# Optimization experiments

Measured on AMD Instinct MI355X. Metric: run time of the kernel, lower is better.

## Reference

```python
import jax, jax.numpy as jnp
import numpy as np

B, A = 65536, 32          # batch, n_agents
D, H1, H2, L = 4, 32, 32, 16  # local MLP dims
G_IN, G_H, G_OUT = 2 * L, 32, 2  # global MLP dims


def _lin_init(k, fan_in, fan_out):
    kw, kb = jax.random.split(k)
    s = 1.0 / np.sqrt(fan_in)
    W = jax.random.uniform(kw, (fan_in, fan_out), minval=-s, maxval=s, dtype=jnp.float32)
    b = jax.random.uniform(kb, (fan_out,), minval=-s, maxval=s, dtype=jnp.float32)
    return W, b


def setup_inputs() -> dict:
    key = jax.random.key(0)
    ks = jax.random.split(key, 9)
    x = jax.random.uniform(ks[0], (B, A * D), dtype=jnp.float32)
    oW1, ob1 = _lin_init(ks[1], D, H1)
    oW2, ob2 = _lin_init(ks[2], H1, H2)
    oW3, ob3 = _lin_init(ks[3], H2, L)
    sW1, sb1 = _lin_init(ks[4], D, H1)
    sW2, sb2 = _lin_init(ks[5], H1, H2)
    sW3, sb3 = _lin_init(ks[6], H2, L)
    gW1, gb1 = _lin_init(ks[7], G_IN, G_H)
    gW2, gb2 = _lin_init(ks[8], G_H, G_OUT)
    return {
        "joint_state_actions": x,
        "selected_agent_idx": 5,
        "oW1": oW1, "ob1": ob1, "oW2": oW2, "ob2": ob2, "oW3": oW3, "ob3": ob3,
        "sW1": sW1, "sb1": sb1, "sW2": sW2, "sb2": sb2, "sW3": sW3, "sb3": sb3,
        "gW1": gW1, "gb1": gb1, "gW2": gW2, "gb2": gb2,
    }


def _mlp3(x, W1, b1, W2, b2, W3, b3):
    h = jax.nn.relu(x @ W1 + b1)
    h = jax.nn.relu(h @ W2 + b2)
    return jax.nn.relu(h @ W3 + b3)


def reference(joint_state_actions, selected_agent_idx,
              oW1, ob1, oW2, ob2, oW3, ob3,
              sW1, sb1, sW2, sb2, sW3, sb3,
              gW1, gb1, gW2, gb2):
    xa = joint_state_actions.reshape(-1, A, D)  # [B, A, 4]
    # other-agents stack applied to all agents at once, masked sum over non-selected
    other = _mlp3(xa, oW1, ob1, oW2, ob2, oW3, ob3)  # [B, A, 16]
    mask = (jnp.arange(A) != selected_agent_idx).astype(other.dtype)[None, :, None]
    sum_other = jnp.sum(other * mask, axis=1)  # [B, 16]
    sel_in = xa[:, selected_agent_idx]  # [B, 4] (static index)
    sel_out = _mlp3(sel_in, sW1, sb1, sW2, sb2, sW3, sb3)  # [B, 16]
    h = jax.nn.relu(jnp.concatenate([sel_out, sum_other], axis=1) @ gW1 + gb1)
    q = h @ gW2 + gb2  # [B, 2]
    actions = sel_in[:, 3].astype(jnp.int32)[:, None]  # [B, 1]
    return jnp.take_along_axis(q, actions, axis=1)  # [B, 1]
```

## Files before the change

kernel.cpp:

```cpp
#include <hip/hip_runtime.h>
#include <hip/hip_bf16.h>

#define DEV __device__ __forceinline__

typedef __attribute__((ext_vector_type(8)))  __bf16    bf16x8;
typedef __attribute__((ext_vector_type(4)))  int       int4v;
typedef __attribute__((ext_vector_type(2)))  unsigned  uint2v;
typedef __attribute__((ext_vector_type(16))) float     vfloat16;

#if __has_builtin(__builtin_amdgcn_permlane32_swap)
#define HAVE_PLSWAP 1
#endif

DEV int pkbf(float a, float b) {
    __hip_bfloat162 h = __float22bfloat162_rn(make_float2(a, b));
    int r;
    __builtin_memcpy(&r, &h, sizeof(r));
    return r;
}

DEV bf16x8 i4_to_frag(int4v v) { return __builtin_bit_cast(bf16x8, v); }

DEV vfloat16 mfma32(bf16x8 a, bf16x8 b, vfloat16 c) {
    return __builtin_amdgcn_mfma_f32_32x32x16_bf16(a, b, c, 0, 0, 0);
}

DEV bf16x8 xposeB(float c0, float c1, float c2, float c3,
                  float c4, float c5, float c6, float c7, bool h) {
    int R0 = pkbf(fmaxf(c0, 0.f), fmaxf(c1, 0.f));
    int R1 = pkbf(fmaxf(c2, 0.f), fmaxf(c3, 0.f));
    int R2 = pkbf(fmaxf(c4, 0.f), fmaxf(c5, 0.f));
    int R3 = pkbf(fmaxf(c6, 0.f), fmaxf(c7, 0.f));
#ifdef HAVE_PLSWAP
    uint2v p0 = __builtin_amdgcn_permlane32_swap((unsigned)R0, (unsigned)R2, false, false);
    uint2v p1 = __builtin_amdgcn_permlane32_swap((unsigned)R1, (unsigned)R3, false, false);
    int4v v;
    v.x = (int)p0.x; v.y = (int)p1.x; v.z = (int)p0.y; v.w = (int)p1.y;
#else
    int S0 = h ? R0 : R2;
    int S1 = h ? R1 : R3;
    int Y0 = __shfl_xor(S0, 32, 64);
    int Y1 = __shfl_xor(S1, 32, 64);
    int4v v;
    v.x = h ? Y0 : R0;
    v.y = h ? Y1 : R1;
    v.z = h ? R2 : Y0;
    v.w = h ? R3 : Y1;
#endif
    return i4_to_frag(v);
}

DEV bf16x8 make_afrag(const float* __restrict__ W, const float* __restrict__ bias,
                      int ld, int Mact, int K, int koff, int lane) {
    int m = lane & 31;
    int h = lane >> 5;
    int d[4];
#pragma unroll
    for (int i = 0; i < 4; ++i) {
        int k0 = koff + h * 8 + 2 * i;
        int k1 = k0 + 1;
        float w0 = 0.f, w1 = 0.f;
        if (m < Mact) {
            if (k0 < K) w0 = W[k0 * ld + m];
            else if (bias && k0 == K) w0 = bias[m];
            if (k1 < K) w1 = W[k1 * ld + m];
            else if (bias && k1 == K) w1 = bias[m];
        }
        d[i] = pkbf(w0, w1);
    }
    int4v v; v.x = d[0]; v.y = d[1]; v.z = d[2]; v.w = d[3];
    return i4_to_frag(v);
}

DEV vfloat16 bvec32(const float* __restrict__ b, int lane) {
    int h = lane >> 5;
    vfloat16 v;
#pragma unroll
    for (int reg = 0; reg < 16; ++reg)
        v[reg] = b[(reg & 3) + 8 * (reg >> 2) + 4 * h];
    return v;
}
DEV vfloat16 bvec16(const float* __restrict__ b, int lane) {
    int h = lane >> 5;
    vfloat16 v;
#pragma unroll
    for (int reg = 0; reg < 16; ++reg)
        v[reg] = (reg < 8) ? b[(reg & 3) + 8 * (reg >> 2) + 4 * h] : 0.f;
    return v;
}

DEV vfloat16 zero16() {
    vfloat16 z;
#pragma unroll
    for (int i = 0; i < 16; ++i) z[i] = 0.f;
    return z;
}

DEV bf16x8 make_b1h(float4 xa, bool h) {
    int4v v;
    v.x = h ? 0 : pkbf(xa.x, xa.y);
    v.y = h ? 0 : pkbf(xa.z, xa.w);
    v.z = h ? 0 : 0x00003f80;
    v.w = 0;
    return i4_to_frag(v);
}

struct Frags {
    bf16x8 A1, A2lo, A2hi, A3lo, A3hi;
    vfloat16 b2, b3;
};

DEV void load_frags(Frags& F,
                    const float* __restrict__ W1, const float* __restrict__ b1,
                    const float* __restrict__ W2, const float* __restrict__ b2,
                    const float* __restrict__ W3, const float* __restrict__ b3,
                    int lane) {
    F.A1   = make_afrag(W1, b1,      32, 32, 4,  0,  lane);
    F.A2lo = make_afrag(W2, nullptr, 32, 32, 32, 0,  lane);
    F.A2hi = make_afrag(W2, nullptr, 32, 32, 32, 16, lane);
    F.A3lo = make_afrag(W3, nullptr, 16, 16, 32, 0,  lane);
    F.A3hi = make_afrag(W3, nullptr, 16, 16, 32, 16, lane);
    F.b2 = bvec32(b2, lane);
    F.b3 = bvec16(b3, lane);
}

DEV vfloat16 run_mlp3(bf16x8 B1, const Frags& F, bool h) {
    vfloat16 C = mfma32(F.A1, B1, zero16());
    bf16x8 Blo = xposeB(C[0], C[1], C[2], C[3], C[4], C[5], C[6], C[7], h);
    bf16x8 Bhi = xposeB(C[8], C[9], C[10], C[11], C[12], C[13], C[14], C[15], h);
    vfloat16 C2 = mfma32(F.A2lo, Blo, F.b2);
    C2 = mfma32(F.A2hi, Bhi, C2);
    Blo = xposeB(C2[0], C2[1], C2[2], C2[3], C2[4], C2[5], C2[6], C2[7], h);
    Bhi = xposeB(C2[8], C2[9], C2[10], C2[11], C2[12], C2[13], C2[14], C2[15], h);
    vfloat16 C3 = mfma32(F.A3lo, Blo, F.b3);
    C3 = mfma32(F.A3hi, Bhi, C3);
    return C3;
}

#define XSTRIDE 132

__global__ __launch_bounds__(256, 4)
void dqn_kernel(const float* __restrict__ x, const int* __restrict__ selp,
                const float* __restrict__ oW1, const float* __restrict__ ob1,
                const float* __restrict__ oW2, const float* __restrict__ ob2,
                const float* __restrict__ oW3, const float* __restrict__ ob3,
                const float* __restrict__ sW1, const float* __restrict__ sb1,
                const float* __restrict__ sW2, const float* __restrict__ sb2,
                const float* __restrict__ sW3, const float* __restrict__ sb3,
                const float* __restrict__ gW1, const float* __restrict__ gb1,
                const float* __restrict__ gW2, const float* __restrict__ gb2,
                float* __restrict__ out)
{
    __shared__ float lds_x[32 * XSTRIDE];
    __shared__ float lds_red[3][8][64];

    const int tid  = threadIdx.x;
    const int lane = tid & 63;
    const int wave = tid >> 6;
    const bool h = lane >= 32;
    const int c = lane & 31;
    const int sel = *selp;
    const int base0 = blockIdx.x * 32;

    {
        const float* xblk = x + (size_t)base0 * 128;
#pragma unroll
        for (int k = 0; k < 4; ++k) {
            int f = tid + 256 * k;
            int row = f >> 5;
            int ag  = f & 31;
            float4 v = *(const float4*)(xblk + (size_t)f * 4);
            *(float4*)&lds_x[ag * XSTRIDE + row * 4] = v;
        }
    }

    Frags Fo;
    load_frags(Fo, oW1, ob1, oW2, ob2, oW3, ob3, lane);

    __syncthreads();

    float sum[8] = {0.f, 0.f, 0.f, 0.f, 0.f, 0.f, 0.f, 0.f};
    const int a0 = wave * 8;

    float4 xa = *(const float4*)&lds_x[a0 * XSTRIDE + c * 4];
#pragma unroll
    for (int a = a0; a < a0 + 8; ++a) {
        int an = (a + 1 < a0 + 8) ? a + 1 : a;
        float4 xn = *(const float4*)&lds_x[an * XSTRIDE + c * 4];
        vfloat16 C3 = run_mlp3(make_b1h(xa, h), Fo, h);
        if (a != sel) {
#pragma unroll
            for (int i = 0; i < 8; ++i) sum[i] += fmaxf(C3[i], 0.f);
        }
        xa = xn;
    }

    if (wave != 0) {
#pragma unroll
        for (int i = 0; i < 8; ++i) lds_red[wave - 1][i][lane] = sum[i];
    }
    __syncthreads();

    if (wave == 0) {
#pragma unroll
        for (int j = 0; j < 3; ++j)
#pragma unroll
            for (int i = 0; i < 8; ++i) sum[i] += lds_red[j][i][lane];

        Frags Fs;
        load_frags(Fs, sW1, sb1, sW2, sb2, sW3, sb3, lane);
        float4 xs = *(const float4*)&lds_x[sel * XSTRIDE + c * 4];
        vfloat16 C3s = run_mlp3(make_b1h(xs, h), Fs, h);

        bf16x8 Ag_lo = make_afrag(gW1, nullptr, 32, 32, 32, 0,  lane);
        bf16x8 Ag_hi = make_afrag(gW1, nullptr, 32, 32, 32, 16, lane);
        vfloat16 gb1v = bvec32(gb1, lane);
        bf16x8 Bg_lo = xposeB(C3s[0], C3s[1], C3s[2], C3s[3],
                              C3s[4], C3s[5], C3s[6], C3s[7], h);
        bf16x8 Bg_hi = xposeB(sum[0], sum[1], sum[2], sum[3],
                              sum[4], sum[5], sum[6], sum[7], h);
        vfloat16 G = mfma32(Ag_lo, Bg_lo, gb1v);
        G = mfma32(Ag_hi, Bg_hi, G);
#pragma unroll
        for (int i = 0; i < 16; ++i) G[i] = fmaxf(G[i], 0.f);

        float q0 = 0.f, q1 = 0.f;
#pragma unroll
        for (int reg = 0; reg < 16; ++reg) {
            int row = (reg & 3) + 8 * (reg >> 2) + (h ? 4 : 0);
            q0 += G[reg] * gW2[row * 2 + 0];
            q1 += G[reg] * gW2[row * 2 + 1];
        }
        q0 += __shfl_xor(q0, 32, 64);
        q1 += __shfl_xor(q1, 32, 64);
        q0 += gb2[0];
        q1 += gb2[1];

        if (!h) {
            int act = (int)xs.w;
            act = act < 0 ? 0 : (act > 1 ? 1 : act);
            out[base0 + c] = act ? q1 : q0;
        }
    }
}

extern "C" void kernel_launch(void* const* d_in, const int* in_sizes, int n_in,
                              void* d_out, int out_size, void* d_ws, size_t ws_size,
                              hipStream_t stream) {
    const float* x   = (const float*)d_in[0];
    const int*   sel = (const int*)d_in[1];
    const float* oW1 = (const float*)d_in[2];
    const float* ob1 = (const float*)d_in[3];
    const float* oW2 = (const float*)d_in[4];
    const float* ob2 = (const float*)d_in[5];
    const float* oW3 = (const float*)d_in[6];
    const float* ob3 = (const float*)d_in[7];
    const float* sW1 = (const float*)d_in[8];
    const float* sb1 = (const float*)d_in[9];
    const float* sW2 = (const float*)d_in[10];
    const float* sb2 = (const float*)d_in[11];
    const float* sW3 = (const float*)d_in[12];
    const float* sb3 = (const float*)d_in[13];
    const float* gW1 = (const float*)d_in[14];
    const float* gb1 = (const float*)d_in[15];
    const float* gW2 = (const float*)d_in[16];
    const float* gb2 = (const float*)d_in[17];
    float* out = (float*)d_out;

    const int B = in_sizes[0] / 128;
    const int blocks = B / 32;
    dqn_kernel<<<blocks, 256, 0, stream>>>(x, sel,
                                           oW1, ob1, oW2, ob2, oW3, ob3,
                                           sW1, sb1, sW2, sb2, sW3, sb3,
                                           gW1, gb1, gW2, gb2, out);
}
```

Measured before the change: 136.9 us.

## Interleave two agents' MLP chains and pre-pack inputs to bf16 in LDS

Processes two agents per loop iteration so the two independent MFMA chains interleave and hide each other's dependency latency. Inputs are converted to bf16 once while staging into LDS, which halves the LDS footprint and the per-agent read width. The bf16 pack now uses a cheap round-half-up and a byte permute instead of the library round-to-nearest-even conversion, and the occupancy hint is dropped from launch_bounds. Side effects: the upper half-wave now also feeds the input data into the B fragment instead of zeros, the action value is re-read from global memory, and bf16 rounding no longer handles ties to even or NaN.

```diff
diff --git a/kernel.cpp b/kernel.cpp
--- a/kernel.cpp
+++ b/kernel.cpp
@@ -13,10 +13,9 @@
 #endif
 
 DEV int pkbf(float a, float b) {
-    __hip_bfloat162 h = __float22bfloat162_rn(make_float2(a, b));
-    int r;
-    __builtin_memcpy(&r, &h, sizeof(r));
-    return r;
+    unsigned ua = __builtin_bit_cast(unsigned, a) + 0x8000u;
+    unsigned ub = __builtin_bit_cast(unsigned, b) + 0x8000u;
+    return (int)__builtin_amdgcn_perm(ua, ub, 0x03020706u);
 }
 
 DEV bf16x8 i4_to_frag(int4v v) { return __builtin_bit_cast(bf16x8, v); }
@@ -96,11 +95,11 @@
     return z;
 }
 
-DEV bf16x8 make_b1h(float4 xa, bool h) {
+DEV bf16x8 b1_from(int2 d) {
     int4v v;
-    v.x = h ? 0 : pkbf(xa.x, xa.y);
-    v.y = h ? 0 : pkbf(xa.z, xa.w);
-    v.z = h ? 0 : 0x00003f80;
+    v.x = d.x;
+    v.y = d.y;
+    v.z = 0x00003f80;
     v.w = 0;
     return i4_to_frag(v);
 }
@@ -125,9 +124,9 @@
 }
 
 DEV vfloat16 run_mlp3(bf16x8 B1, const Frags& F, bool h) {
-    vfloat16 C = mfma32(F.A1, B1, zero16());
-    bf16x8 Blo = xposeB(C[0], C[1], C[2], C[3], C[4], C[5], C[6], C[7], h);
-    bf16x8 Bhi = xposeB(C[8], C[9], C[10], C[11], C[12], C[13], C[14], C[15], h);
+    vfloat16 C1 = mfma32(F.A1, B1, zero16());
+    bf16x8 Blo = xposeB(C1[0], C1[1], C1[2], C1[3], C1[4], C1[5], C1[6], C1[7], h);
+    bf16x8 Bhi = xposeB(C1[8], C1[9], C1[10], C1[11], C1[12], C1[13], C1[14], C1[15], h);
     vfloat16 C2 = mfma32(F.A2lo, Blo, F.b2);
     C2 = mfma32(F.A2hi, Bhi, C2);
     Blo = xposeB(C2[0], C2[1], C2[2], C2[3], C2[4], C2[5], C2[6], C2[7], h);
@@ -137,9 +136,9 @@
     return C3;
 }
 
-#define XSTRIDE 132
-
-__global__ __launch_bounds__(256, 4)
+#define XSTRIDE 66
+
+__global__ __launch_bounds__(256)
 void dqn_kernel(const float* __restrict__ x, const int* __restrict__ selp,
                 const float* __restrict__ oW1, const float* __restrict__ ob1,
                 const float* __restrict__ oW2, const float* __restrict__ ob2,
@@ -151,7 +150,7 @@
                 const float* __restrict__ gW2, const float* __restrict__ gb2,
                 float* __restrict__ out)
 {
-    __shared__ float lds_x[32 * XSTRIDE];
+    __shared__ int   lds_xb[32 * XSTRIDE];
     __shared__ float lds_red[3][8][64];
 
     const int tid  = threadIdx.x;
@@ -170,7 +169,10 @@
             int row = f >> 5;
             int ag  = f & 31;
             float4 v = *(const float4*)(xblk + (size_t)f * 4);
-            *(float4*)&lds_x[ag * XSTRIDE + row * 4] = v;
+            int2 d;
+            d.x = pkbf(v.x, v.y);
+            d.y = pkbf(v.z, v.w);
+            *(int2*)&lds_xb[ag * XSTRIDE + row * 2] = d;
         }
     }
 
@@ -181,18 +183,44 @@
 
     float sum[8] = {0.f, 0.f, 0.f, 0.f, 0.f, 0.f, 0.f, 0.f};
     const int a0 = wave * 8;
-
-    float4 xa = *(const float4*)&lds_x[a0 * XSTRIDE + c * 4];
-#pragma unroll
-    for (int a = a0; a < a0 + 8; ++a) {
-        int an = (a + 1 < a0 + 8) ? a + 1 : a;
-        float4 xn = *(const float4*)&lds_x[an * XSTRIDE + c * 4];
-        vfloat16 C3 = run_mlp3(make_b1h(xa, h), Fo, h);
-        if (a != sel) {
-#pragma unroll
-            for (int i = 0; i < 8; ++i) sum[i] += fmaxf(C3[i], 0.f);
-        }
-        xa = xn;
+    const int* xb = &lds_xb[a0 * XSTRIDE + c * 2];
+
+#pragma unroll
+    for (int i = 0; i < 8; i += 2) {
+        int2 da = *(const int2*)(xb + i * XSTRIDE);
+        int2 db = *(const int2*)(xb + (i + 1) * XSTRIDE);
+
+        vfloat16 C1a = mfma32(Fo.A1, b1_from(da), zero16());
+        vfloat16 C1b = mfma32(Fo.A1, b1_from(db), zero16());
+
+        bf16x8 Bal = xposeB(C1a[0], C1a[1], C1a[2], C1a[3], C1a[4], C1a[5], C1a[6], C1a[7], h);
+        bf16x8 Bbl = xposeB(C1b[0], C1b[1], C1b[2], C1b[3], C1b[4], C1b[5], C1b[6], C1b[7], h);
+        bf16x8 Bah = xposeB(C1a[8], C1a[9], C1a[10], C1a[11], C1a[12], C1a[13], C1a[14], C1a[15], h);
+        bf16x8 Bbh = xposeB(C1b[8], C1b[9], C1b[10], C1b[11], C1b[12], C1b[13], C1b[14], C1b[15], h);
+
+        vfloat16 C2a = mfma32(Fo.A2lo, Bal, Fo.b2);
+        vfloat16 C2b = mfma32(Fo.A2lo, Bbl, Fo.b2);
+        C2a = mfma32(Fo.A2hi, Bah, C2a);
+        C2b = mfma32(Fo.A2hi, Bbh, C2b);
+
+        Bal = xposeB(C2a[0], C2a[1], C2a[2], C2a[3], C2a[4], C2a[5], C2a[6], C2a[7], h);
+        Bbl = xposeB(C2b[0], C2b[1], C2b[2], C2b[3], C2b[4], C2b[5], C2b[6], C2b[7], h);
+        Bah = xposeB(C2a[8], C2a[9], C2a[10], C2a[11], C2a[12], C2a[13], C2a[14], C2a[15], h);
+        Bbh = xposeB(C2b[8], C2b[9], C2b[10], C2b[11], C2b[12], C2b[13], C2b[14], C2b[15], h);
+
+        vfloat16 C3a = mfma32(Fo.A3lo, Bal, Fo.b3);
+        vfloat16 C3b = mfma32(Fo.A3lo, Bbl, Fo.b3);
+        C3a = mfma32(Fo.A3hi, Bah, C3a);
+        C3b = mfma32(Fo.A3hi, Bbh, C3b);
+
+        if (a0 + i != sel) {
+#pragma unroll
+            for (int j = 0; j < 8; ++j) sum[j] += fmaxf(C3a[j], 0.f);
+        }
+        if (a0 + i + 1 != sel) {
+#pragma unroll
+            for (int j = 0; j < 8; ++j) sum[j] += fmaxf(C3b[j], 0.f);
+        }
     }
 
     if (wave != 0) {
@@ -209,8 +237,8 @@
 
         Frags Fs;
         load_frags(Fs, sW1, sb1, sW2, sb2, sW3, sb3, lane);
-        float4 xs = *(const float4*)&lds_x[sel * XSTRIDE + c * 4];
-        vfloat16 C3s = run_mlp3(make_b1h(xs, h), Fs, h);
+        int2 ds = *(const int2*)&lds_xb[sel * XSTRIDE + c * 2];
+        vfloat16 C3s = run_mlp3(b1_from(ds), Fs, h);
 
         bf16x8 Ag_lo = make_afrag(gW1, nullptr, 32, 32, 32, 0,  lane);
         bf16x8 Ag_hi = make_afrag(gW1, nullptr, 32, 32, 32, 16, lane);
@@ -237,7 +265,8 @@
         q1 += gb2[1];
 
         if (!h) {
-            int act = (int)xs.w;
+            float f3 = x[(size_t)(base0 + c) * 128 + sel * 4 + 3];
+            int act = (int)f3;
             act = act < 0 ? 0 : (act > 1 ? 1 : act);
             out[base0 + c] = act ? q1 : q0;
         }
```

Measured after the change: 135.2 us. About the same (-1.2%).
